# Kernel optimization log

Hardware: AMD Instinct MI355X
Metric: run time of the kernel (lower is better)

Reference implementation:

```python
import jax, jax.numpy as jnp
import numpy as np

N_NODES = 32768
N_GRAPHS = 16
N_PER = N_NODES // N_GRAPHS  # 2048 nodes per graph
N_EDGES = 262144
D = 128      # node_state_dim
DE = 64      # edge_state_dim
H = 256      # edge hidden / message dim (= 2*D, required by matching prop)
NH = 256     # node MLP hidden


def _mlp2(x, W1, b1, W2, b2):
    # Linear -> ReLU -> Linear (torch nn.Linear convention: y = x @ W.T + b)
    return jax.nn.relu(x @ W1.T + b1) @ W2.T + b2


def setup_inputs() -> dict:
    key = jax.random.key(0)
    ks = jax.random.split(key, 16)
    s = 0.1  # edge_net_init_scale-ish small init
    inp = {
        "node_states": jax.random.normal(ks[0], (N_NODES, D), jnp.float32),
        "edge_features": jax.random.normal(ks[1], (N_EDGES, DE), jnp.float32),
        "from_idx": jax.random.randint(ks[2], (N_EDGES,), 0, N_NODES, jnp.int32),
        "to_idx": jax.random.randint(ks[3], (N_EDGES,), 0, N_NODES, jnp.int32),
        "graph_idx": jnp.repeat(jnp.arange(N_GRAPHS, dtype=jnp.int32), N_PER),
        "n_graphs": N_GRAPHS,
        # forward message net: Linear(2D+DE -> H), Linear(H -> H)
        "Wm1": jax.random.normal(ks[4], (H, 2 * D + DE), jnp.float32) * s,
        "bm1": jnp.zeros((H,), jnp.float32),
        "Wm2": jax.random.normal(ks[5], (H, H), jnp.float32) * s,
        "bm2": jnp.zeros((H,), jnp.float32),
        # reverse message net (separate params)
        "Wr1": jax.random.normal(ks[6], (H, 2 * D + DE), jnp.float32) * s,
        "br1": jnp.zeros((H,), jnp.float32),
        "Wr2": jax.random.normal(ks[7], (H, H), jnp.float32) * s,
        "br2": jnp.zeros((H,), jnp.float32),
        # node update MLP: Linear(4D -> NH), Linear(NH -> D)
        "Wn1": jax.random.normal(ks[8], (NH, 4 * D), jnp.float32) * s,
        "bn1": jnp.zeros((NH,), jnp.float32),
        "Wn2": jax.random.normal(ks[9], (D, NH), jnp.float32) * s,
        "bn2": jnp.zeros((D,), jnp.float32),
    }
    return inp


def _forward(node_states, edge_features, from_idx, to_idx, n_graphs,
             Wm1, bm1, Wm2, bm2, Wr1, br1, Wr2, br2, Wn1, bn1, Wn2, bn2):
    n = node_states.shape[0]
    fs = node_states[from_idx]   # [E, D] gather
    ts = node_states[to_idx]     # [E, D]
    # forward direction: messages -> scatter-add into to_idx
    m_fwd = _mlp2(jnp.concatenate([fs, ts, edge_features], -1), Wm1, bm1, Wm2, bm2)
    agg = jax.ops.segment_sum(m_fwd, to_idx, num_segments=n)
    # reverse direction: swap endpoints, scatter-add into from_idx
    m_rev = _mlp2(jnp.concatenate([ts, fs, edge_features], -1), Wr1, br1, Wr2, br2)
    agg = agg + jax.ops.segment_sum(m_rev, from_idx, num_segments=n)

    # cross-graph dual-softmax attention over (i, i+1) graph pairs.
    # graph_idx is contiguous equal-size blocks -> reshape partitioning.
    n_per = n // n_graphs
    d = node_states.reshape(n_graphs // 2, 2, n_per, -1)
    x, y = d[:, 0], d[:, 1]                      # [P, Np, D] each
    a = jnp.einsum('pid,pjd->pij', x, y)         # dotproduct similarity
    a_x = jax.nn.softmax(a, axis=2)              # softmax over y per x-row
    a_y = jax.nn.softmax(a, axis=1)              # softmax over x per y-col
    attn_x = jnp.einsum('pij,pjd->pid', a_x, y)  # [P, Np, D]
    attn_y = jnp.einsum('pij,pid->pjd', a_y, x)  # [P, Np, D]
    cross = jnp.stack([attn_x, attn_y], axis=1).reshape(n, -1)

    attention_input = node_states - cross
    node_inputs = jnp.concatenate([agg, attention_input, node_states], -1)  # [N, 4D]
    mlp_out = _mlp2(node_inputs, Wn1, bn1, Wn2, bn2)
    return node_states + mlp_out  # residual update


def reference(node_states, edge_features, from_idx, to_idx, graph_idx, n_graphs,
              Wm1, bm1, Wm2, bm2, Wr1, br1, Wr2, br2, Wn1, bn1, Wn2, bn2):
    return _forward(node_states, edge_features, from_idx, to_idx, int(n_graphs),
                    Wm1, bm1, Wm2, bm2, Wr1, br1, Wr2, br2, Wn1, bn1, Wn2, bn2)
```

## Files before the change

### kernel.cpp

```cpp
#include <hip/hip_runtime.h>


typedef __bf16 bf16_t;
typedef __bf16 bf16x8 __attribute__((ext_vector_type(8)));
typedef __bf16 bf16x4 __attribute__((ext_vector_type(4)));
typedef float  f32x4  __attribute__((ext_vector_type(4)));

#define MFMA16(a,b,c) __builtin_amdgcn_mfma_f32_16x16x32_bf16((a),(b),(c),0,0,0)

constexpr int NNODES = 32768;
constexpr int NEDGES = 262144;
constexpr int DD = 128;
constexpr int HH = 256;

__device__ __forceinline__ bf16x8 cvt8(f32x4 a, f32x4 b){
  bf16x8 r;
  r[0]=(bf16_t)a[0]; r[1]=(bf16_t)a[1]; r[2]=(bf16_t)a[2]; r[3]=(bf16_t)a[3];
  r[4]=(bf16_t)b[0]; r[5]=(bf16_t)b[1]; r[6]=(bf16_t)b[2]; r[7]=(bf16_t)b[3];
  return r;
}

__global__ void pack_weights_kernel(const float* __restrict__ Wm1, const float* __restrict__ Wr1,
                                    const float* __restrict__ Wn2,
                                    bf16_t* __restrict__ wp, bf16_t* __restrict__ wc,
                                    bf16_t* __restrict__ wn2){
  const int bx = blockIdx.x;
  const int tid = threadIdx.x;
  if (bx < 128){
    int idx = (bx*256 + tid)*4;
    int n = idx >> 7, k = idx & 127;
    const float* W = (n < 512) ? Wm1 : Wr1;
    int row = n & 255;
    int colbase = ((n >> 8) & 1) * 128;
    f32x4 v = *(const f32x4*)(W + (size_t)row*320 + colbase + k);
    bf16x4 o; o[0]=(bf16_t)v[0]; o[1]=(bf16_t)v[1]; o[2]=(bf16_t)v[2]; o[3]=(bf16_t)v[3];
    *(bf16x4*)(wp + idx) = o;
  } else if (bx < 144){
    int g = (bx-128)*256 + tid;
    int part = g >> 11, gg = g & 2047;
    int tile = gg >> 6, lane = gg & 63;
    int kc = tile >> 4, nt = tile & 15;
    int lr = lane & 15, lk = lane >> 4;
    const float* W = part ? Wr1 : Wm1;
    int row = nt*16 + lr;
    int col = 256 + kc*32 + lk*8;
    f32x4 v0 = *(const f32x4*)(W + (size_t)row*320 + col);
    f32x4 v1 = *(const f32x4*)(W + (size_t)row*320 + col + 4);
    *(bf16x8*)(wc + (size_t)g*8) = cvt8(v0,v1);
  } else {
    int g = (bx-144)*256 + tid;
    int tile = g >> 6, lane = g & 63;
    int kc = tile >> 3, nt = tile & 7;
    int lr = lane & 15, lk = lane >> 4;
    int row = nt*16 + lr;
    int col = kc*32 + lk*8;
    f32x4 v0 = *(const f32x4*)(Wn2 + (size_t)row*256 + col);
    f32x4 v1 = *(const f32x4*)(Wn2 + (size_t)row*256 + col + 4);
    *(bf16x8*)(wn2 + (size_t)g*8) = cvt8(v0,v1);
  }
}

__global__ void hist_kernel(const int* __restrict__ to_idx, const int* __restrict__ from_idx,
                            int* __restrict__ cnt_to, int* __restrict__ cnt_from){
  int e = blockIdx.x*256 + threadIdx.x;
  if (e < NEDGES){
    atomicAdd(&cnt_to[to_idx[e]], 1);
    atomicAdd(&cnt_from[from_idx[e]], 1);
  }
}

__global__ void scan_kernel(int* __restrict__ cnt_to, int* __restrict__ cnt_from,
                            int* __restrict__ start_to, int* __restrict__ start_from){
  int* cnt   = blockIdx.x ? cnt_from : cnt_to;
  int* start = blockIdx.x ? start_from : start_to;
  __shared__ int sums[1024];
  const int t = threadIdx.x;
  int local[32]; int s = 0;
  #pragma unroll
  for (int j=0;j<32;j++){ local[j] = cnt[t*32+j]; s += local[j]; }
  sums[t] = s; __syncthreads();
  #pragma unroll
  for (int d=1; d<1024; d<<=1){
    int v = (t>=d) ? sums[t-d] : 0;
    __syncthreads();
    sums[t] += v;
    __syncthreads();
  }
  int off = sums[t] - s;
  #pragma unroll
  for (int j=0;j<32;j++){
    start[t*32+j] = off;
    cnt[t*32+j]   = off;
    off += local[j];
  }
  if (t == 1023) start[32768] = sums[1023];
}

__global__ void place_kernel(const int* __restrict__ to_idx, const int* __restrict__ from_idx,
                             int* __restrict__ cur_to, int* __restrict__ cur_from,
                             int* __restrict__ eid_to, int* __restrict__ eid_from,
                             int* __restrict__ rowv_to, int* __restrict__ rowv_from){
  int e = blockIdx.x*256 + threadIdx.x;
  if (e < NEDGES){
    int vt = to_idx[e];
    int p = atomicAdd(&cur_to[vt], 1);
    eid_to[p] = e;
    rowv_to[p] = vt;
    int vf = from_idx[e];
    int q = atomicAdd(&cur_from[vf], 1);
    eid_from[q] = e;
    rowv_from[q] = vf;
  }
}

__global__ __launch_bounds__(256,3) void proj_kernel(
    const float* __restrict__ ns, const bf16_t* __restrict__ Wp,
    const float* __restrict__ bm1, const float* __restrict__ br1,
    bf16_t* __restrict__ P1f, bf16_t* __restrict__ P2f,
    bf16_t* __restrict__ P1r, bf16_t* __restrict__ P2r)
{
  constexpr int XS = 136;
  constexpr int CS = 264;
  __shared__ bf16_t Xs[64*XS];
  __shared__ bf16_t Cs[64*CS];
  const int tid = threadIdx.x;
  const int rb = blockIdx.x*64;
  const int cb = blockIdx.y;
  const int dir = blockIdx.z;
  const float* bvec = dir ? br1 : bm1;
  #pragma unroll
  for (int it=0; it<8; ++it){
    int c = tid + it*256;
    int row = c >> 5, co = (c & 31)*4;
    f32x4 v = *(const f32x4*)(ns + (size_t)(rb+row)*DD + co);
    bf16x4 o; o[0]=(bf16_t)v[0]; o[1]=(bf16_t)v[1]; o[2]=(bf16_t)v[2]; o[3]=(bf16_t)v[3];
    *(bf16x4*)&Xs[row*XS + co] = o;
  }
  __syncthreads();
  const int lane = tid & 63, wave = tid >> 6, lr = lane & 15, lk = lane >> 4;
  const bf16_t* Wb = Wp + (size_t)(dir*2 + cb)*32768;
  f32x4 acc[16];
  #pragma unroll
  for (int nt=0;nt<16;nt++) acc[nt] = (f32x4){0.f,0.f,0.f,0.f};
  #pragma unroll
  for (int kc=0;kc<4;kc++){
    bf16x8 a = *(const bf16x8*)&Xs[(wave*16 + lr)*XS + kc*32 + lk*8];
    #pragma unroll
    for (int nt=0;nt<16;nt++){
      bf16x8 b = *(const bf16x8*)&Wb[(size_t)(nt*16 + lr)*128 + kc*32 + lk*8];
      acc[nt] = MFMA16(a,b,acc[nt]);
    }
  }
  #pragma unroll
  for (int nt=0;nt<16;nt++){
    const float bias = cb ? bvec[nt*16 + lr] : 0.f;
    #pragma unroll
    for (int r=0;r<4;r++)
      Cs[(wave*16 + lk*4 + r)*CS + nt*16 + lr] = (bf16_t)(acc[nt][r] + bias);
  }
  __syncthreads();
  bf16_t* P = dir ? (cb ? P2r : P1r) : (cb ? P2f : P1f);
  #pragma unroll
  for (int it=0; it<8; ++it){
    int c = tid + it*256;
    int row = c >> 5, co = (c & 31)*8;
    *(bf16x8*)&P[(size_t)(rb+row)*HH + co] = *(const bf16x8*)&Cs[row*CS + co];
  }
}

__global__ __launch_bounds__(256,4) void edge_agg_kernel(
    const float* __restrict__ ef, const bf16_t* __restrict__ Wc,
    const int* __restrict__ eid_to, const int* __restrict__ eid_from,
    const int* __restrict__ from_idx, const int* __restrict__ to_idx,
    const int* __restrict__ rowv_to, const int* __restrict__ rowv_from,
    const int* __restrict__ start_to, const int* __restrict__ start_from,
    const bf16_t* __restrict__ P1f, const bf16_t* __restrict__ P2f,
    const bf16_t* __restrict__ P1r, const bf16_t* __restrict__ P2r,
    bf16_t* __restrict__ partial_f, bf16_t* __restrict__ partial_r,
    bf16_t* __restrict__ aggh_f, bf16_t* __restrict__ aggh_r)
{
  constexpr int CS = 264;
  __shared__ bf16_t Cs[64*CS];
  __shared__ int es[64], os[64], vs[64];
  const int tid = threadIdx.x;
  const int dir = blockIdx.x >> 12;
  const int rb = (blockIdx.x & 4095)*64;
  const int* eid  = dir ? eid_from  : eid_to;
  const int* oth  = dir ? to_idx    : from_idx;
  const int* rowv = dir ? rowv_from : rowv_to;
  const int* start= dir ? start_from: start_to;
  const bf16_t* P1 = dir ? P1r : P1f;
  const bf16_t* P2 = dir ? P2r : P2f;
  bf16_t* partial  = dir ? partial_r : partial_f;
  bf16_t* aggh     = dir ? aggh_r : aggh_f;
  const bf16_t* Wcd = Wc + (size_t)dir*16384;

  if (tid < 64){
    int e = eid[rb + tid];
    es[tid] = e;
    os[tid] = oth[e];
    vs[tid] = rowv[rb + tid];
  }
  __syncthreads();

  const int lane = tid & 63, wave = tid >> 6, lr = lane & 15, lk = lane >> 4;
  {
    const float* arow = ef + (size_t)es[wave*16 + lr]*64;
    bf16x8 a0, a1;
    {
      f32x4 v0 = *(const f32x4*)(arow + lk*8);
      f32x4 v1 = *(const f32x4*)(arow + lk*8 + 4);
      a0 = cvt8(v0,v1);
      f32x4 w0 = *(const f32x4*)(arow + 32 + lk*8);
      f32x4 w1 = *(const f32x4*)(arow + 32 + lk*8 + 4);
      a1 = cvt8(w0,w1);
    }
    #pragma unroll
    for (int p=0;p<2;p++){
      f32x4 acc[8];
      #pragma unroll
      for (int nt=0;nt<8;nt++) acc[nt] = (f32x4){0.f,0.f,0.f,0.f};
      #pragma unroll
      for (int nt=0;nt<8;nt++){
        bf16x8 b0 = *(const bf16x8*)&Wcd[(size_t)((0*16 + p*8 + nt)*64 + lane)*8];
        acc[nt] = MFMA16(a0,b0,acc[nt]);
        bf16x8 b1v = *(const bf16x8*)&Wcd[(size_t)((1*16 + p*8 + nt)*64 + lane)*8];
        acc[nt] = MFMA16(a1,b1v,acc[nt]);
      }
      #pragma unroll
      for (int nt=0;nt<8;nt++)
        #pragma unroll
        for (int r=0;r<4;r++)
          Cs[(wave*16 + lk*4 + r)*CS + (p*8+nt)*16 + lr] = (bf16_t)acc[nt][r];
    }
  }
  __syncthreads();

  const int c8 = (tid & 31) * 8;
  const int rbase = (tid >> 5) * 8;
  {
    #pragma unroll
    for (int j=0;j<8;j++){
      const int row = rbase + j;
      bf16x8 cs = *(const bf16x8*)&Cs[row*CS + c8];
      bf16x8 p1 = *(const bf16x8*)&P1[(size_t)os[row]*HH + c8];
      bf16x8 p2 = *(const bf16x8*)&P2[(size_t)vs[row]*HH + c8];
      bf16x8 o;
      #pragma unroll
      for (int k=0;k<8;k++)
        o[k] = (bf16_t)fmaxf((float)cs[k] + (float)p1[k] + (float)p2[k], 0.f);
      *(bf16x8*)&Cs[row*CS + c8] = o;
    }
  }
  __syncthreads();

  const int c = tid;
  float runsum = 0.f;
  int curv = vs[0];
  for (int row=0; row<64; ++row){
    const int v = vs[row];
    if (v != curv){
      const int s0 = start[curv], s1 = start[curv+1];
      if (s0 >= rb && s1 <= rb+64)
        aggh[(size_t)curv*HH + c] = (bf16_t)runsum;
      else
        partial[((size_t)curv*2 + (s0 >= rb ? 0 : 1))*HH + c] = (bf16_t)runsum;
      runsum = 0.f; curv = v;
    }
    runsum += (float)Cs[row*CS + c];
  }
  {
    const int s0 = start[curv], s1 = start[curv+1];
    if (s0 >= rb && s1 <= rb+64)
      aggh[(size_t)curv*HH + c] = (bf16_t)runsum;
    else
      partial[((size_t)curv*2 + (s0 >= rb ? 0 : 1))*HH + c] = (bf16_t)runsum;
  }
}

__global__ __launch_bounds__(256) void combine_kernel(
    const bf16_t* __restrict__ partial_f, const bf16_t* __restrict__ partial_r,
    const int* __restrict__ start_to, const int* __restrict__ start_from,
    bf16_t* __restrict__ aggh_f, bf16_t* __restrict__ aggh_r)
{
  const int dir = blockIdx.y;
  const bf16_t* partial = dir ? partial_r : partial_f;
  const int* start = dir ? start_from : start_to;
  bf16_t* aggh = dir ? aggh_r : aggh_f;
  const int tid = threadIdx.x;
  const int v = blockIdx.x*8 + (tid>>5);
  const int c0 = (tid & 31)*8;
  const int s0 = start[v], s1 = start[v+1];
  if (s1 == s0){
    bf16x8 z;
    #pragma unroll
    for (int j=0;j<8;j++) z[j] = (bf16_t)0.f;
    *(bf16x8*)&aggh[(size_t)v*HH + c0] = z;
  } else if ((s0>>6) != ((s1-1)>>6)){
    bf16x8 a = *(const bf16x8*)&partial[((size_t)v*2    )*HH + c0];
    bf16x8 b = *(const bf16x8*)&partial[((size_t)v*2 + 1)*HH + c0];
    bf16x8 o;
    #pragma unroll
    for (int j=0;j<8;j++) o[j] = (bf16_t)((float)a[j] + (float)b[j]);
    *(bf16x8*)&aggh[(size_t)v*HH + c0] = o;
  }
}

__global__ __launch_bounds__(256) void w2t_uw_kernel(const float* __restrict__ Wm2, const float* __restrict__ Wr2,
                                                     bf16_t* __restrict__ wm2T, bf16_t* __restrict__ wr2T,
                                                     const float* __restrict__ Wn1,
                                                     const float* __restrict__ bm2, const float* __restrict__ br2,
                                                     float* __restrict__ u, float* __restrict__ w){
  if (blockIdx.x == 32){
    const int n = threadIdx.x;
    float su=0.f, sw=0.f;
    for (int j=0;j<256;j+=4){
      f32x4 wv = *(const f32x4*)(Wn1 + (size_t)n*512 + j);
      f32x4 bu = *(const f32x4*)(bm2 + j);
      f32x4 bw = *(const f32x4*)(br2 + j);
      #pragma unroll
      for (int q=0;q<4;q++){ su += wv[q]*bu[q]; sw += wv[q]*bw[q]; }
    }
    u[n]=su; w[n]=sw;
    return;
  }
  __shared__ bf16_t t[64][72];
  const int bi = (blockIdx.x & 3)*64;
  const int bj = ((blockIdx.x>>2) & 3)*64;
  const int m  = blockIdx.x >> 4;
  const float* W = m ? Wr2 : Wm2;
  bf16_t* WT = m ? wr2T : wm2T;
  const int tid = threadIdx.x;
  #pragma unroll
  for (int it=0; it<16; ++it){
    int c = tid + it*256;
    int r = c >> 6, co = c & 63;
    t[r][co] = (bf16_t)W[(size_t)(bi+r)*256 + bj + co];
  }
  __syncthreads();
  #pragma unroll
  for (int it=0; it<16; ++it){
    int c = tid + it*256;
    int r = c >> 6, co = c & 63;
    WT[(size_t)(bj+r)*256 + bi + co] = t[co][r];
  }
}

__global__ __launch_bounds__(256,2) void wcat_gemm_kernel(
    const float* __restrict__ Wn1, const bf16_t* __restrict__ wm2T, const bf16_t* __restrict__ wr2T,
    bf16_t* __restrict__ wcat)
{
  constexpr int XS = 264, CS = 264;
  const int tid = threadIdx.x;
  const int cb = blockIdx.y;
  if (cb == 2){
    #pragma unroll
    for (int it=0; it<8; ++it){
      int g = blockIdx.x*2048 + it*256 + tid;
      int tile = g >> 6, lane = g & 63;
      int kc = tile >> 4, nt = tile & 15;
      int lr = lane & 15, lk = lane >> 4;
      int row = nt*16 + lr;
      int col = 256 + kc*32 + lk*8;
      f32x4 v0 = *(const f32x4*)(Wn1 + (size_t)row*512 + col);
      f32x4 v1 = *(const f32x4*)(Wn1 + (size_t)row*512 + col + 4);
      *(bf16x8*)&wcat[(size_t)(((16 + kc)*16 + nt)*64 + lane)*8] = cvt8(v0,v1);
    }
    return;
  }
  __shared__ bf16_t Xs[64*XS];
  __shared__ bf16_t Cs[64*CS];
  const int rb = blockIdx.x*64;
  const bf16_t* BT = cb ? wr2T : wm2T;
  #pragma unroll
  for (int it=0; it<16; ++it){
    int c = tid + it*256;
    int row = c >> 6, co = (c & 63)*4;
    f32x4 v = *(const f32x4*)(Wn1 + (size_t)(rb+row)*512 + co);
    bf16x4 o; o[0]=(bf16_t)v[0]; o[1]=(bf16_t)v[1]; o[2]=(bf16_t)v[2]; o[3]=(bf16_t)v[3];
    *(bf16x4*)&Xs[row*XS + co] = o;
  }
  __syncthreads();
  const int lane = tid & 63, wave = tid >> 6, lr = lane & 15, lk = lane >> 4;
  f32x4 acc[16];
  #pragma unroll
  for (int nt=0;nt<16;nt++) acc[nt] = (f32x4){0.f,0.f,0.f,0.f};
  #pragma unroll
  for (int kc=0;kc<8;kc++){
    bf16x8 a = *(const bf16x8*)&Xs[(wave*16 + lr)*XS + kc*32 + lk*8];
    #pragma unroll
    for (int nt=0;nt<16;nt++){
      bf16x8 b = *(const bf16x8*)&BT[(size_t)(nt*16 + lr)*256 + kc*32 + lk*8];
      acc[nt] = MFMA16(a,b,acc[nt]);
    }
  }
  #pragma unroll
  for (int nt=0;nt<16;nt++)
    #pragma unroll
    for (int r=0;r<4;r++)
      Cs[(wave*16 + lk*4 + r)*CS + nt*16 + lr] = (bf16_t)acc[nt][r];
  __syncthreads();
  const int nt_base = rb >> 4;
  #pragma unroll
  for (int it=0; it<8; ++it){
    int g = tid + it*256;
    int tile = g >> 6, lane2 = g & 63;
    int kc_l = tile >> 2, nt_l = tile & 3;
    int lr2 = lane2 & 15, lk2 = lane2 >> 4;
    bf16x8 v = *(const bf16x8*)&Cs[(nt_l*16 + lr2)*CS + kc_l*32 + lk2*8];
    *(bf16x8*)&wcat[(size_t)(((cb*8 + kc_l)*16 + nt_base + nt_l)*64 + lane2)*8] = v;
  }
}

__global__ __launch_bounds__(256) void nst_kernel(const float* __restrict__ ns,
                                                  bf16_t* __restrict__ nsT,
                                                  bf16_t* __restrict__ nsB){
  constexpr int XS2 = 136;
  __shared__ bf16_t Xs[64*XS2];
  const int tid = threadIdx.x;
  const int nb = blockIdx.x*64;
  #pragma unroll
  for (int it=0; it<8; ++it){
    int c = tid + it*256;
    int rowl = c >> 5, co = (c & 31)*4;
    f32x4 v = *(const f32x4*)(ns + (size_t)(nb+rowl)*DD + co);
    bf16x4 o; o[0]=(bf16_t)v[0]; o[1]=(bf16_t)v[1]; o[2]=(bf16_t)v[2]; o[3]=(bf16_t)v[3];
    *(bf16x4*)&Xs[rowl*XS2 + co] = o;
    *(bf16x4*)&nsB[(size_t)(nb+rowl)*DD + co] = o;
  }
  __syncthreads();
  const int sb = nb >> 11;
  const int jb = nb & 2047;
  bf16_t* outp = nsT + (size_t)sb*DD*2048 + jb;
  #pragma unroll
  for (int it=0; it<4; ++it){
    int c = tid + it*256;
    int d = c >> 3, g8 = (c & 7)*8;
    bf16x8 o;
    #pragma unroll
    for (int k=0;k<8;k++){
      int s64 = g8 + k;
      int t32 = s64 >> 5, s = s64 & 31;
      int m = (s & 1) ? (16 + (s>>1)) : (s>>1);
      o[k] = Xs[(t32*32 + m)*XS2 + d];
    }
    *(bf16x8*)(outp + (size_t)d*2048 + g8) = o;
  }
}

__global__ __launch_bounds__(256,3) void attn_kernel(
    const bf16_t* __restrict__ nsB, const bf16_t* __restrict__ nsT,
    float* __restrict__ Opart, float* __restrict__ lpart)
{
  constexpr int KS = 136;
  constexpr int VS = 40;
  constexpr int PS = 40;
  __shared__ bf16_t Ks[2][32*KS];
  __shared__ bf16_t Vt[2][128*VS];
  __shared__ bf16_t Ps[64*PS];
  const int tid = threadIdx.x;
  const int lane = tid & 63, wave = tid >> 6, lr = lane & 15, lk = lane >> 4;
  const int bx = blockIdx.x;
  const int qt = bx & 31, side = (bx>>5)&1, p = (bx>>6)&7, kvh = bx>>9;
  const size_t qbase = (size_t)p*4096 + (size_t)side*2048 + (size_t)qt*64;
  const int sbkv = p*2 + (side^1);
  const bf16_t* Kv = nsB + ((size_t)p*4096 + (size_t)(side^1)*2048)*DD + (size_t)kvh*32*32*DD;
  const bf16_t* Vp = nsT + (size_t)sbkv*DD*2048 + (size_t)kvh*32*32;

  bf16x8 qf[4];
  {
    const bf16_t* qrow = nsB + (qbase + wave*16 + lr)*DD;
    #pragma unroll
    for (int kc=0;kc<4;kc++) qf[kc] = *(const bf16x8*)(qrow + kc*32 + lk*8);
  }
  float ls[4] = {0.f,0.f,0.f,0.f};
  f32x4 acco[8];
  #pragma unroll
  for (int nt=0;nt<8;nt++) acco[nt]=(f32x4){0.f,0.f,0.f,0.f};

  const int krow0 = tid>>4,        kcol = (tid&15)*8;
  const int vd0   = tid>>2,        vsl  = (tid&3)*8;
  bf16x8 kreg0, kreg1, vreg0, vreg1;

  auto load_tile = [&](int t){
    const bf16_t* kp = Kv + (size_t)t*32*DD;
    kreg0 = *(const bf16x8*)(kp + (size_t)krow0*DD + kcol);
    kreg1 = *(const bf16x8*)(kp + (size_t)(krow0+16)*DD + kcol);
    const bf16_t* vp = Vp + t*32;
    vreg0 = *(const bf16x8*)(vp + (size_t)vd0*2048 + vsl);
    vreg1 = *(const bf16x8*)(vp + (size_t)(vd0+64)*2048 + vsl);
  };
  auto store_tile = [&](int b){
    *(bf16x8*)&Ks[b][krow0*KS + kcol]      = kreg0;
    *(bf16x8*)&Ks[b][(krow0+16)*KS + kcol] = kreg1;
    *(bf16x8*)&Vt[b][vd0*VS + vsl]         = vreg0;
    *(bf16x8*)&Vt[b][(vd0+64)*VS + vsl]    = vreg1;
  };

  load_tile(0);
  store_tile(0);
  load_tile(1);
  __syncthreads();
  int cur = 0;
  for (int t=0; t<32; ++t){
    if (t+1 < 32){
      store_tile(cur^1);
      if (t+2 < 32) load_tile(t+2);
    }
    f32x4 s0 = (f32x4){0.f,0.f,0.f,0.f}, s1 = (f32x4){0.f,0.f,0.f,0.f};
    #pragma unroll
    for (int kc=0;kc<4;kc++){
      bf16x8 b0 = *(const bf16x8*)&Ks[cur][lr*KS      + kc*32 + lk*8];
      bf16x8 b1 = *(const bf16x8*)&Ks[cur][(16+lr)*KS + kc*32 + lk*8];
      s0 = MFMA16(qf[kc], b0, s0);
      s1 = MFMA16(qf[kc], b1, s1);
    }
    #pragma unroll
    for (int r=0;r<4;r++){
      float p0 = __expf(s0[r] - 40.f);
      float p1 = __expf(s1[r] - 40.f);
      ls[r] += p0 + p1;
      union { bf16_t h[2]; unsigned u; } pk;
      pk.h[0] = (bf16_t)p0; pk.h[1] = (bf16_t)p1;
      *(unsigned*)&Ps[(wave*16 + lk*4 + r)*PS + 2*lr] = pk.u;
    }
    asm volatile("s_waitcnt lgkmcnt(0)" ::: "memory");
    __builtin_amdgcn_sched_barrier(0);
    bf16x8 pa = *(const bf16x8*)&Ps[(wave*16 + lr)*PS + lk*8];
    #pragma unroll
    for (int nt=0;nt<8;nt++){
      bf16x8 vb = *(const bf16x8*)&Vt[cur][(nt*16+lr)*VS + lk*8];
      acco[nt] = MFMA16(pa, vb, acco[nt]);
    }
    __syncthreads();
    cur ^= 1;
  }
  #pragma unroll
  for (int r=0;r<4;r++){
    float v = ls[r];
    v += __shfl_xor(v,1); v += __shfl_xor(v,2);
    v += __shfl_xor(v,4); v += __shfl_xor(v,8);
    ls[r] = v;
  }
  float* Op = Opart + (size_t)kvh*NNODES*DD;
  #pragma unroll
  for (int r=0;r<4;r++){
    const size_t row = qbase + wave*16 + lk*4 + r;
    if (lr == 0) lpart[(size_t)kvh*NNODES + row] = ls[r];
    #pragma unroll
    for (int nt=0;nt<8;nt++)
      Op[row*DD + nt*16 + lr] = acco[nt][r];
  }
}

__global__ __launch_bounds__(256) void attn_combine_kernel(
    const float* __restrict__ ns, const float* __restrict__ Opart,
    const float* __restrict__ lpart, bf16_t* __restrict__ attnB)
{
  const int tid = threadIdx.x;
  const int row = blockIdx.x*16 + (tid >> 4);
  const int c0 = (tid & 15)*8;
  const float inv = 1.f/(lpart[row] + lpart[NNODES + row]);
  const float* o0 = Opart + (size_t)row*DD + c0;
  const float* o1 = Opart + (size_t)NNODES*DD + (size_t)row*DD + c0;
  const float* nr = ns + (size_t)row*DD + c0;
  f32x4 a0 = *(const f32x4*)o0,      a1 = *(const f32x4*)(o0+4);
  f32x4 b0 = *(const f32x4*)o1,      b1 = *(const f32x4*)(o1+4);
  f32x4 n0 = *(const f32x4*)nr,      n1 = *(const f32x4*)(nr+4);
  bf16x8 o;
  #pragma unroll
  for (int j=0;j<4;j++){
    o[j]   = (bf16_t)(n0[j] - (a0[j]+b0[j])*inv);
    o[4+j] = (bf16_t)(n1[j] - (a1[j]+b1[j])*inv);
  }
  *(bf16x8*)&attnB[(size_t)row*DD + c0] = o;
}

__global__ __launch_bounds__(256,2) void node_mlp_kernel(
    const bf16_t* __restrict__ agghf, const bf16_t* __restrict__ agghr,
    const bf16_t* __restrict__ attnB, const bf16_t* __restrict__ nsB,
    const float* __restrict__ ns,
    const bf16_t* __restrict__ wcat, const float* __restrict__ bn1,
    const float* __restrict__ uvec, const float* __restrict__ wvec,
    const int* __restrict__ start_to, const int* __restrict__ start_from,
    const bf16_t* __restrict__ Wn2b, const float* __restrict__ bn2,
    float* __restrict__ out)
{
  __shared__ __align__(16) bf16_t As[32*768];
  bf16_t* Hs = As;
  const int tid = threadIdx.x;
  const int lane = tid & 63, wave = tid >> 6, lr = lane & 15, lk = lane >> 4;
  const int rb = blockIdx.x*32;

  bf16x8 stg[12];
  int dsta[12];
  #pragma unroll
  for (int it=0; it<12; ++it){
    const int db = it*4096 + tid*16;
    const int row = db / 1536;
    const int within = db - row*1536;
    const size_t node = (size_t)(rb + row);
    const char* s0 = (const char*)agghf + (node<<9) + within;
    const char* s1 = (const char*)agghr + (node<<9) + (within-512);
    const char* s2 = (const char*)attnB + (node<<8) + (within-1024);
    const char* s3 = (const char*)nsB   + (node<<8) + (within-1280);
    const char* src = within < 512 ? s0 : (within < 1024 ? s1 : (within < 1280 ? s2 : s3));
    stg[it] = *(const bf16x8*)src;
    dsta[it] = row*1536 + (within ^ ((row & 7) << 4));
  }
  #pragma unroll
  for (int it=0; it<12; ++it)
    *(bf16x8*)((char*)As + dsta[it]) = stg[it];
  __syncthreads();

  const int cg = wave >> 1;
  const int colbase = cg * 128;
  const int arow = (wave & 1)*16 + lr;
  const unsigned abase = (unsigned)arow * 1536u;
  const unsigned asw = ((unsigned)(arow & 7)) << 4;
  f32x4 acc[8];
  #pragma unroll
  for (int nt=0;nt<8;nt++) acc[nt] = (f32x4){0.f,0.f,0.f,0.f};
  #pragma unroll
  for (int kc=0; kc<24; ++kc){
    const unsigned y = (unsigned)(kc*64 + lk*16);
    bf16x8 a = *(const bf16x8*)((const char*)As + abase + (y ^ asw));
    #pragma unroll
    for (int nt=0;nt<8;nt++){
      bf16x8 b = *(const bf16x8*)&wcat[(size_t)((kc*16 + cg*8 + nt)*64 + lane)*8];
      acc[nt] = MFMA16(a,b,acc[nt]);
    }
  }
  __syncthreads();

  const int r0 = rb + (wave&1)*16 + lk*4;
  float dt[4], df[4];
  #pragma unroll
  for (int r=0;r<4;r++){
    dt[r] = (float)(start_to[r0+r+1]   - start_to[r0+r]);
    df[r] = (float)(start_from[r0+r+1] - start_from[r0+r]);
  }
  #pragma unroll
  for (int nt=0;nt<8;nt++){
    const int col = colbase + nt*16 + lr;
    const float bias = bn1[col];
    const float uu = uvec[col], ww = wvec[col];
    #pragma unroll
    for (int r=0;r<4;r++){
      float v = acc[nt][r] + bias + dt[r]*uu + df[r]*ww;
      v = v > 0.f ? v : 0.f;
      Hs[((wave&1)*16 + lk*4 + r)*264 + col] = (bf16_t)v;
    }
  }
  __syncthreads();

  const int cb2 = cg * 64;
  f32x4 acc2[4];
  #pragma unroll
  for (int nt=0;nt<4;nt++) acc2[nt] = (f32x4){0.f,0.f,0.f,0.f};
  #pragma unroll
  for (int kc=0;kc<8;kc++){
    bf16x8 a = *(const bf16x8*)&Hs[((wave&1)*16 + lr)*264 + kc*32 + lk*8];
    #pragma unroll
    for (int nt=0;nt<4;nt++){
      bf16x8 b = *(const bf16x8*)&Wn2b[(size_t)((kc*8 + cg*4 + nt)*64 + lane)*8];
      acc2[nt] = MFMA16(a,b,acc2[nt]);
    }
  }
  #pragma unroll
  for (int nt=0;nt<4;nt++){
    const int col = cb2 + nt*16 + lr;
    const float bias = bn2[col];
    #pragma unroll
    for (int r=0;r<4;r++){
      const size_t rr = (size_t)(r0 + r);
      out[rr*DD + col] = acc2[nt][r] + bias + ns[rr*DD + col];
    }
  }
}

extern "C" void kernel_launch(void* const* d_in, const int* in_sizes, int n_in,
                              void* d_out, int out_size, void* d_ws, size_t ws_size,
                              hipStream_t stream) {
  const float* ns  = (const float*)d_in[0];
  const float* ef  = (const float*)d_in[1];
  const int* from_idx = (const int*)d_in[2];
  const int* to_idx   = (const int*)d_in[3];
  const float* Wm1 = (const float*)d_in[6];  const float* bm1 = (const float*)d_in[7];
  const float* Wm2 = (const float*)d_in[8];  const float* bm2 = (const float*)d_in[9];
  const float* Wr1 = (const float*)d_in[10]; const float* br1 = (const float*)d_in[11];
  const float* Wr2 = (const float*)d_in[12]; const float* br2 = (const float*)d_in[13];
  const float* Wn1 = (const float*)d_in[14]; const float* bn1 = (const float*)d_in[15];
  const float* Wn2 = (const float*)d_in[16]; const float* bn2 = (const float*)d_in[17];

  char* ws = (char*)d_ws;
  bf16_t* partial_f = (bf16_t*)(ws);
  bf16_t* partial_r = (bf16_t*)(ws + 33554432);
  int*    rowv_to   = (int*)(ws + 67108864);
  int*    rowv_from = (int*)(ws + 68157440);
  bf16_t* P1r   = (bf16_t*)(ws + 69206016);
  bf16_t* P2r   = (bf16_t*)(ws + 85983232);
  bf16_t* P1f   = (bf16_t*)(ws + 134217728);
  bf16_t* P2f   = (bf16_t*)(ws + 150994944);
  bf16_t* aggh_f = (bf16_t*)(ws + 167772160);
  bf16_t* aggh_r = (bf16_t*)(ws + 184549376);
  bf16_t* wpb  = (bf16_t*)(ws + 201326592);
  bf16_t* wcb  = (bf16_t*)(ws + 201588736);
  bf16_t* wn2b = (bf16_t*)(ws + 201654272);
  int* cur_to     = (int*)(ws + 202244096);
  int* cur_from   = (int*)(ws + 202375168);
  int* start_to   = (int*)(ws + 202506240);
  int* start_from = (int*)(ws + 202637320);
  int* eid_to     = (int*)(ws + 202768400);
  int* eid_from   = (int*)(ws + 203816976);
  bf16_t* attnB = (bf16_t*)(ws);
  bf16_t* nsB   = (bf16_t*)(ws + 33554432);
  bf16_t* nsT   = (bf16_t*)(ws + 41943040);
  bf16_t* wm2T  = (bf16_t*)(ws + 50331648);
  bf16_t* wr2T  = (bf16_t*)(ws + 50462720);
  bf16_t* wcat  = (bf16_t*)(ws + 50593792);
  float*  uvec  = (float*) (ws + 50987008);
  float*  wvec  = (float*) (ws + 50988032);
  float*  Opart = (float*) (ws + 69206016);
  float*  lpart = (float*) (ws + 102760448);

  hipMemsetAsync(cur_to, 0, 2*NNODES*sizeof(int), stream);

  pack_weights_kernel<<<160, 256, 0, stream>>>(Wm1, Wr1, Wn2, wpb, wcb, wn2b);

  hist_kernel<<<NEDGES/256, 256, 0, stream>>>(to_idx, from_idx, cur_to, cur_from);
  scan_kernel<<<2, 1024, 0, stream>>>(cur_to, cur_from, start_to, start_from);
  place_kernel<<<NEDGES/256, 256, 0, stream>>>(to_idx, from_idx, cur_to, cur_from,
      eid_to, eid_from, rowv_to, rowv_from);

  proj_kernel<<<dim3(NNODES/64, 2, 2), 256, 0, stream>>>(ns, wpb, bm1, br1,
      P1f, P2f, P1r, P2r);

  edge_agg_kernel<<<2*NEDGES/64, 256, 0, stream>>>(ef, wcb,
      eid_to, eid_from, from_idx, to_idx, rowv_to, rowv_from, start_to, start_from,
      P1f, P2f, P1r, P2r, partial_f, partial_r, aggh_f, aggh_r);

  combine_kernel<<<dim3(NNODES/8, 2), 256, 0, stream>>>(partial_f, partial_r,
      start_to, start_from, aggh_f, aggh_r);

  nst_kernel<<<NNODES/64, 256, 0, stream>>>(ns, nsT, nsB);
  w2t_uw_kernel<<<33, 256, 0, stream>>>(Wm2, Wr2, wm2T, wr2T, Wn1, bm2, br2, uvec, wvec);
  wcat_gemm_kernel<<<dim3(4,3), 256, 0, stream>>>(Wn1, wm2T, wr2T, wcat);

  attn_kernel<<<1024, 256, 0, stream>>>(nsB, nsT, Opart, lpart);
  attn_combine_kernel<<<NNODES/16, 256, 0, stream>>>(ns, Opart, lpart, attnB);

  node_mlp_kernel<<<NNODES/32, 256, 0, stream>>>(aggh_f, aggh_r, attnB, nsB, ns,
      wcat, bn1, uvec, wvec, start_to, start_from, wn2b, bn2, (float*)d_out);
}
```

Measured before the change: 412.4 us.

## Pre-convert edge features to bf16, compact partial buffers by tile, raise node MLP occupancy

The histogram kernel now also converts edge features from fp32 to bf16 once, so the edge aggregation kernel gathers half as many bytes per edge in each of its two direction passes. The per-node partial-sum buffers are re-indexed by edge tile instead of by node, which shrinks them and lets the workspace be repacked. The combine kernel reads the boundary partials from adjacent tiles. Separately, node_mlp launch bounds are raised to 3 blocks per CU, which may force register spills.

After: 423.7 us. 1.03x slower.

```diff
diff --git a/kernel.cpp b/kernel.cpp
--- a/kernel.cpp
+++ b/kernel.cpp
@@ -61,11 +61,19 @@
 }
 
 __global__ void hist_kernel(const int* __restrict__ to_idx, const int* __restrict__ from_idx,
-                            int* __restrict__ cnt_to, int* __restrict__ cnt_from){
-  int e = blockIdx.x*256 + threadIdx.x;
-  if (e < NEDGES){
-    atomicAdd(&cnt_to[to_idx[e]], 1);
-    atomicAdd(&cnt_from[from_idx[e]], 1);
+                            int* __restrict__ cnt_to, int* __restrict__ cnt_from,
+                            const float* __restrict__ ef, bf16_t* __restrict__ efB){
+  const int tid = threadIdx.x;
+  int e = blockIdx.x*256 + tid;
+  atomicAdd(&cnt_to[to_idx[e]], 1);
+  atomicAdd(&cnt_from[from_idx[e]], 1);
+  const size_t cbase = (size_t)blockIdx.x * 16384;
+  #pragma unroll
+  for (int it=0; it<8; ++it){
+    size_t i = cbase + (size_t)it*2048 + (size_t)tid*8;
+    f32x4 v0 = *(const f32x4*)(ef + i);
+    f32x4 v1 = *(const f32x4*)(ef + i + 4);
+    *(bf16x8*)(efB + i) = cvt8(v0,v1);
   }
 }
 
@@ -169,7 +177,7 @@
 }
 
 __global__ __launch_bounds__(256,4) void edge_agg_kernel(
-    const float* __restrict__ ef, const bf16_t* __restrict__ Wc,
+    const bf16_t* __restrict__ efB, const bf16_t* __restrict__ Wc,
     const int* __restrict__ eid_to, const int* __restrict__ eid_from,
     const int* __restrict__ from_idx, const int* __restrict__ to_idx,
     const int* __restrict__ rowv_to, const int* __restrict__ rowv_from,
@@ -184,7 +192,8 @@
   __shared__ int es[64], os[64], vs[64];
   const int tid = threadIdx.x;
   const int dir = blockIdx.x >> 12;
-  const int rb = (blockIdx.x & 4095)*64;
+  const int tile = blockIdx.x & 4095;
+  const int rb = tile*64;
   const int* eid  = dir ? eid_from  : eid_to;
   const int* oth  = dir ? to_idx    : from_idx;
   const int* rowv = dir ? rowv_from : rowv_to;
@@ -205,16 +214,9 @@
 
   const int lane = tid & 63, wave = tid >> 6, lr = lane & 15, lk = lane >> 4;
   {
-    const float* arow = ef + (size_t)es[wave*16 + lr]*64;
-    bf16x8 a0, a1;
-    {
-      f32x4 v0 = *(const f32x4*)(arow + lk*8);
-      f32x4 v1 = *(const f32x4*)(arow + lk*8 + 4);
-      a0 = cvt8(v0,v1);
-      f32x4 w0 = *(const f32x4*)(arow + 32 + lk*8);
-      f32x4 w1 = *(const f32x4*)(arow + 32 + lk*8 + 4);
-      a1 = cvt8(w0,w1);
-    }
+    const bf16_t* arow = efB + (size_t)es[wave*16 + lr]*64;
+    bf16x8 a0 = *(const bf16x8*)(arow + lk*8);
+    bf16x8 a1 = *(const bf16x8*)(arow + 32 + lk*8);
     #pragma unroll
     for (int p=0;p<2;p++){
       f32x4 acc[8];
@@ -264,7 +266,7 @@
       if (s0 >= rb && s1 <= rb+64)
         aggh[(size_t)curv*HH + c] = (bf16_t)runsum;
       else
-        partial[((size_t)curv*2 + (s0 >= rb ? 0 : 1))*HH + c] = (bf16_t)runsum;
+        partial[((size_t)tile*2 + (s0 >= rb ? 1 : 0))*HH + c] = (bf16_t)runsum;
       runsum = 0.f; curv = v;
     }
     runsum += (float)Cs[row*CS + c];
@@ -274,7 +276,7 @@
     if (s0 >= rb && s1 <= rb+64)
       aggh[(size_t)curv*HH + c] = (bf16_t)runsum;
     else
-      partial[((size_t)curv*2 + (s0 >= rb ? 0 : 1))*HH + c] = (bf16_t)runsum;
+      partial[((size_t)tile*2 + (s0 >= rb ? 1 : 0))*HH + c] = (bf16_t)runsum;
   }
 }
 
@@ -297,8 +299,9 @@
     for (int j=0;j<8;j++) z[j] = (bf16_t)0.f;
     *(bf16x8*)&aggh[(size_t)v*HH + c0] = z;
   } else if ((s0>>6) != ((s1-1)>>6)){
-    bf16x8 a = *(const bf16x8*)&partial[((size_t)v*2    )*HH + c0];
-    bf16x8 b = *(const bf16x8*)&partial[((size_t)v*2 + 1)*HH + c0];
+    const int t0 = s0 >> 6;
+    bf16x8 a = *(const bf16x8*)&partial[((size_t)t0*2 + 1)*HH + c0];
+    bf16x8 b = *(const bf16x8*)&partial[((size_t)(t0+1)*2 + 0)*HH + c0];
     bf16x8 o;
     #pragma unroll
     for (int j=0;j<8;j++) o[j] = (bf16_t)((float)a[j] + (float)b[j]);
@@ -576,7 +579,7 @@
   *(bf16x8*)&attnB[(size_t)row*DD + c0] = o;
 }
 
-__global__ __launch_bounds__(256,2) void node_mlp_kernel(
+__global__ __launch_bounds__(256,3) void node_mlp_kernel(
     const bf16_t* __restrict__ agghf, const bf16_t* __restrict__ agghr,
     const bf16_t* __restrict__ attnB, const bf16_t* __restrict__ nsB,
     const float* __restrict__ ns,
@@ -695,11 +698,12 @@
 
   char* ws = (char*)d_ws;
   bf16_t* partial_f = (bf16_t*)(ws);
-  bf16_t* partial_r = (bf16_t*)(ws + 33554432);
-  int*    rowv_to   = (int*)(ws + 67108864);
-  int*    rowv_from = (int*)(ws + 68157440);
-  bf16_t* P1r   = (bf16_t*)(ws + 69206016);
-  bf16_t* P2r   = (bf16_t*)(ws + 85983232);
+  bf16_t* partial_r = (bf16_t*)(ws + 4194304);
+  bf16_t* efB       = (bf16_t*)(ws + 8388608);
+  int*    rowv_to   = (int*)(ws + 41943040);
+  int*    rowv_from = (int*)(ws + 42991616);
+  bf16_t* P1r   = (bf16_t*)(ws + 44040192);
+  bf16_t* P2r   = (bf16_t*)(ws + 60817408);
   bf16_t* P1f   = (bf16_t*)(ws + 134217728);
   bf16_t* P2f   = (bf16_t*)(ws + 150994944);
   bf16_t* aggh_f = (bf16_t*)(ws + 167772160);
@@ -728,7 +732,7 @@
 
   pack_weights_kernel<<<160, 256, 0, stream>>>(Wm1, Wr1, Wn2, wpb, wcb, wn2b);
 
-  hist_kernel<<<NEDGES/256, 256, 0, stream>>>(to_idx, from_idx, cur_to, cur_from);
+  hist_kernel<<<NEDGES/256, 256, 0, stream>>>(to_idx, from_idx, cur_to, cur_from, ef, efB);
   scan_kernel<<<2, 1024, 0, stream>>>(cur_to, cur_from, start_to, start_from);
   place_kernel<<<NEDGES/256, 256, 0, stream>>>(to_idx, from_idx, cur_to, cur_from,
       eid_to, eid_from, rowv_to, rowv_from);
@@ -736,7 +740,7 @@
   proj_kernel<<<dim3(NNODES/64, 2, 2), 256, 0, stream>>>(ns, wpb, bm1, br1,
       P1f, P2f, P1r, P2r);
 
-  edge_agg_kernel<<<2*NEDGES/64, 256, 0, stream>>>(ef, wcb,
+  edge_agg_kernel<<<2*NEDGES/64, 256, 0, stream>>>(efB, wcb,
       eid_to, eid_from, from_idx, to_idx, rowv_to, rowv_from, start_to, start_from,
       P1f, P2f, P1r, P2r, partial_f, partial_r, aggh_f, aggh_r);
 
```
